# Kernel optimization log

Measured on AMD Instinct MI355X. Metric: run time of the kernel, lower is better.

The kernel has to match this reference:

```python
import jax, jax.numpy as jnp
import numpy as np

B, H, W = 16, 256, 256
C = 64          # width
M1, M2 = 12, 12 # retained Fourier modes
FC_HID = 128


def setup_inputs() -> dict:
    key = jax.random.key(0)
    ks = jax.random.split(key, 10)
    scale = 1.0 / (C * C)
    inp = {
        "x": jax.random.normal(ks[0], (B, H, W, 1), dtype=jnp.float32),
        "fc0_w": jax.random.normal(ks[1], (1, C), dtype=jnp.float32) * (1.0 / np.sqrt(1)),
        "fc0_b": jnp.zeros((C,), dtype=jnp.float32),
        # 4 layers x {weights1, weights2} x [Cin, Cout, M1, M2] x {re, im}
        "sc_w": jax.random.uniform(ks[2], (4, 2, C, C, M1, M2, 2), dtype=jnp.float32) * scale,
        # 1x1 conv weights [layer, Cout, Cin] and biases [layer, Cout]
        "pw_w": jax.random.normal(ks[3], (4, C, C), dtype=jnp.float32) * (1.0 / np.sqrt(C)),
        "pw_b": jnp.zeros((4, C), dtype=jnp.float32),
        "fc1_w": jax.random.normal(ks[4], (C, FC_HID), dtype=jnp.float32) * (1.0 / np.sqrt(C)),
        "fc1_b": jnp.zeros((FC_HID,), dtype=jnp.float32),
        "fc2_w": jax.random.normal(ks[5], (FC_HID, 1), dtype=jnp.float32) * (1.0 / np.sqrt(FC_HID)),
        "fc2_b": jnp.zeros((1,), dtype=jnp.float32),
    }
    return inp


def _spectral_conv(x, w1, w2):
    # x: [B, C, H, W] real; w1, w2: [Cin, Cout, M1, M2] complex
    xf = jnp.fft.rfft2(x, axes=(-2, -1))                # [B, C, H, W//2+1]
    top = jnp.einsum('bixy,ioxy->boxy', xf[:, :, :M1, :M2], w1)
    bot = jnp.einsum('bixy,ioxy->boxy', xf[:, :, -M1:, :M2], w2)
    out_ft = jnp.zeros((x.shape[0], w1.shape[1], x.shape[2], x.shape[3] // 2 + 1),
                       dtype=jnp.complex64)
    out_ft = out_ft.at[:, :, :M1, :M2].set(top)
    out_ft = out_ft.at[:, :, -M1:, :M2].set(bot)
    return jnp.fft.irfft2(out_ft, s=(x.shape[2], x.shape[3]), axes=(-2, -1))


def _gelu(x):
    return jax.nn.gelu(x, approximate=False)  # torch F.gelu default = exact erf


def reference(x, fc0_w, fc0_b, sc_w, pw_w, pw_b, fc1_w, fc1_b, fc2_w, fc2_b):
    # lift: [B,H,W,1] -> [B,H,W,C] -> [B,C,H,W]
    h = jnp.einsum('bhwi,ic->bhwc', x, fc0_w) + fc0_b
    h = jnp.transpose(h, (0, 3, 1, 2))
    scw = sc_w[..., 0] + 1j * sc_w[..., 1]  # [4, 2, C, C, M1, M2] complex
    for l in range(4):
        x1 = _spectral_conv(h, scw[l, 0], scw[l, 1])
        x2 = jnp.einsum('bihw,oi->bohw', h, pw_w[l]) + pw_b[l][None, :, None, None]
        h = x1 + x2
        if l < 3:
            h = _gelu(h)
    h = jnp.transpose(h, (0, 2, 3, 1))  # [B,H,W,C]
    h = _gelu(jnp.einsum('bhwc,cd->bhwd', h, fc1_w) + fc1_b)
    out = jnp.einsum('bhwd,do->bhwo', h, fc2_w) + fc2_b
    return out
```

## Files before the change

### kernel.cpp

```cpp
#include <hip/hip_runtime.h>
#include <hip/hip_bf16.h>
#include <math.h>

#define Hn 256
#define Wn 256
#define Cn 64
#define Mk 12
#define NM 24
#define FCH 128
#define HW 65536

using half8 = __attribute__((ext_vector_type(8))) _Float16;
using f32x4 = __attribute__((ext_vector_type(4))) float;

__device__ __forceinline__ float gelu_exact(float x) {
    return 0.5f * x * (1.0f + erff(x * 0.7071067811865476f));
}
__device__ __forceinline__ unsigned short f2h(float f) {
    _Float16 h = (_Float16)f;
    return __builtin_bit_cast(unsigned short, h);
}
__device__ __forceinline__ float h2lo(unsigned u) {
    return (float)__builtin_bit_cast(_Float16, (unsigned short)(u & 0xffffu));
}
__device__ __forceinline__ float h2hi(unsigned u) {
    return (float)__builtin_bit_cast(_Float16, (unsigned short)(u >> 16));
}

__global__ __launch_bounds__(256) void k_init_tables(float* tc, float* ts,
                                                     float* twc, float* tws,
                                                     float* tcs,
                                                     unsigned short* bfr,
                                                     unsigned short* tfr) {
    int i = threadIdx.x;
    const float step = 0.024543692606170259f;
    float c = cosf(i * step), s = sinf(i * step);
    tc[i] = c; ts[i] = s;
    tcs[2 * i] = c; tcs[2 * i + 1] = s;
    for (int k = 0; k < Mk; ++k) {
        int idx = (i * k) & 255;
        twc[i * Mk + k] = cosf(idx * step);
        tws[i * Mk + k] = sinf(idx * step);
    }
    for (int e = i; e < 8192; e += 256) {
        int j  = e & 7;
        int l  = (e >> 3) & 63;
        int sn = e >> 9;
        int col = (sn & 1) * 16 + (l & 15);
        int ky = col >> 1, p = col & 1;
        int k  = (sn >> 1) * 32 + ((l >> 4) & 3) * 8 + j;
        int idx = (ky * k) & 255;
        float v = p ? -sinf(idx * step) : cosf(idx * step);
        bfr[e] = f2h(v);
    }
    for (int e = i; e < 12288; e += 256) {
        int j  = e & 7;
        int l  = (e >> 3) & 63;
        int sm = e >> 9;
        int mt = sm % 3, s2 = sm / 3;
        int r  = mt * 16 + (l & 15);
        int hh = s2 * 32 + ((l >> 4) & 3) * 8 + j;
        int m  = (r < 24) ? r : (r - 24);
        int kx = (m < Mk) ? m : (232 + m);
        int idx = (kx * hh) & 255;
        float v = (r < 24) ? cosf(idx * step) : sinf(idx * step);
        tfr[e] = f2h(v);
    }
}

__global__ __launch_bounds__(256) void k_prep_frag(const float* __restrict__ pww,
                                                   const float* __restrict__ fc1w,
                                                   unsigned short* __restrict__ efr,
                                                   unsigned short* __restrict__ pwfr,
                                                   unsigned short* __restrict__ fc1fr) {
    int e = blockIdx.x * 256 + threadIdx.x;
    const float step = 0.024543692606170259f;
    int j = e & 7, l = (e >> 3) & 63;
    int row = l & 15;
    int k = ((l >> 4) & 3) * 8 + j;
    if (e < 8192) {
        int mt = (e >> 9) & 15;
        int pix = mt * 16 + row;
        float v = 0.f;
        if (k < 12) v = cosf(((k * pix) & 255) * step);
        else if (k < 24) v = -sinf((((k - 12) * pix) & 255) * step);
        efr[e] = f2h(v);
    } else if (e < 24576) {
        int e2 = e - 8192;
        int nt = (e2 >> 9) & 3;
        int ks = (e2 >> 11) & 1;
        int l4 = e2 >> 12;
        int o = nt * 16 + row;
        int i = ks * 32 + k;
        pwfr[e2] = f2h(pww[(size_t)(l4 * 64 + o) * 64 + i]);
    } else {
        int e2 = e - 24576;
        int nt = (e2 >> 9) & 7;
        int ks = (e2 >> 12) & 1;
        int d = nt * 16 + row;
        int i = ks * 32 + k;
        fc1fr[e2] = f2h(fc1w[i * 128 + d]);
    }
}

__global__ __launch_bounds__(256) void k_prep_w(const float* __restrict__ scw,
                                                float* __restrict__ scwT) {
    int t = blockIdx.x * 256 + threadIdx.x;
    int o  = t & 63;
    int i  = (t >> 6) & 63;
    int r  = t >> 12;
    int u  = r % 6;
    int kx = (r / 6) % 12;
    int lj = r / 72;
    int ky = 2 * u;
    size_t in_idx = ((((size_t)lj * 64 + i) * 64 + o) * 144) + kx * Mk + ky;
    float4 v = *(const float4*)(scw + 2 * in_idx);
    size_t o0 = ((((size_t)(lj * 12 + kx) * Mk + ky) * 64 + i) * 64 + o);
    size_t o1 = ((((size_t)(lj * 12 + kx) * Mk + ky + 1) * 64 + i) * 64 + o);
    *(float2*)(scwT + 2 * o0) = make_float2(v.x, v.y);
    *(float2*)(scwT + 2 * o1) = make_float2(v.z, v.w);
}

__global__ __launch_bounds__(256) void k_prep_wfrag(const float* __restrict__ scwT,
                                                    unsigned short* __restrict__ wfr) {
    __shared__ float Ws[8192];
    int mat = blockIdx.x;
    int t = threadIdx.x;
    const float4* src = (const float4*)(scwT + (size_t)mat * 8192);
#pragma unroll
    for (int r = 0; r < 8; ++r)
        ((float4*)Ws)[r * 256 + t] = src[r * 256 + t];
    __syncthreads();
    unsigned short* dst = wfr + (size_t)mat * 16384;
#pragma unroll
    for (int u = 0; u < 8; ++u) {
        int lin = u * 256 + t;
        int lane = lin & 63, nt = (lin >> 6) & 7, s = lin >> 9;
        int col = nt * 16 + (lane & 15);
        int o = col >> 1, pp = col & 1;
        int tg = (lane >> 4) & 3;
        unsigned pk[4];
#pragma unroll
        for (int jp = 0; jp < 4; ++jp) {
            unsigned short hv[2];
#pragma unroll
            for (int hz = 0; hz < 2; ++hz) {
                int k = s * 32 + tg * 8 + jp * 2 + hz;
                int i = k >> 1, p = k & 1;
                float wr_ = Ws[(i * 64 + o) * 2];
                float wi_ = Ws[(i * 64 + o) * 2 + 1];
                float v = (p == 0) ? (pp == 0 ? wr_ : wi_)
                                   : (pp == 0 ? -wi_ : wr_);
                hv[hz] = f2h(v);
            }
            pk[jp] = hv[0] | ((unsigned)hv[1] << 16);
        }
        uint4 w4 = {pk[0], pk[1], pk[2], pk[3]};
        *(uint4*)(dst + lin * 8) = w4;
    }
}

__global__ __launch_bounds__(64) void k_dftw_x(const float* __restrict__ x,
                                               float* __restrict__ Xxw,
                                               const float* __restrict__ twc,
                                               const float* __restrict__ tws) {
    int r = blockIdx.x * 64 + threadIdx.x;
    const float* hp = x + (size_t)r * Wn;
    float xr[Mk], xi[Mk];
#pragma unroll
    for (int k = 0; k < Mk; ++k) { xr[k] = 0.f; xi[k] = 0.f; }
    for (int w4 = 0; w4 < 64; ++w4) {
        float4 v = ((const float4*)hp)[w4];
        float vv[4] = {v.x, v.y, v.z, v.w};
#pragma unroll
        for (int j = 0; j < 4; ++j) {
            int wbase = (w4 * 4 + j) * Mk;
#pragma unroll
            for (int k = 0; k < Mk; ++k) {
                xr[k] += vv[j] * twc[wbase + k];
                xi[k] -= vv[j] * tws[wbase + k];
            }
        }
    }
    float* op = Xxw + (size_t)r * (2 * Mk);
#pragma unroll
    for (int k = 0; k < Mk; ++k) { op[2 * k] = xr[k]; op[2 * k + 1] = xi[k]; }
}

__global__ __launch_bounds__(256) void k_xdfth(const float* __restrict__ Xxw,
                                               float* __restrict__ Xfx,
                                               const float* __restrict__ tc,
                                               const float* __restrict__ ts) {
    int t = blockIdx.x * 256 + threadIdx.x;
    if (t >= 16 * 288) return;
    int ky = t % Mk;
    int m  = (t / Mk) % NM;
    int b  = t / 288;
    int kx = (m < Mk) ? m : (232 + m);
    const float* base = Xxw + (size_t)b * Hn * 2 * Mk + 2 * ky;
    float ar = 0.f, ai = 0.f;
    for (int hh = 0; hh < Hn; ++hh) {
        float vr = base[hh * 2 * Mk];
        float vi = base[hh * 2 * Mk + 1];
        int idx = (kx * hh) & 255;
        float c = tc[idx], s = ts[idx];
        ar += vr * c + vi * s;
        ai += vi * c - vr * s;
    }
    Xfx[2 * t] = ar;
    Xfx[2 * t + 1] = ai;
}

__global__ __launch_bounds__(256) void k_mixZ2(const float* __restrict__ xin,
                                               const unsigned short* __restrict__ wfr,
                                               const float* __restrict__ w0,
                                               const float* __restrict__ b0v,
                                               float* __restrict__ Z,
                                               int l, int first, int b0, int bc) {
    __shared__ __align__(16) char smem[4096];
    int t = threadIdx.x;
    int lane = t & 63, q = t >> 6, tg = (lane >> 4) & 3;
    int blk = blockIdx.x;
    int jj = blk / 144, kxw = (blk / 12) % 12, ky = blk % 12;
    int mm = jj * 12 + kxw;
    int mk = mm * 12 + ky;
    int mat = (l * 2 + jj) * 144 + kxw * 12 + ky;
    {
        int b = t >> 4, c16 = t & 15;
        uint4 pk = {0u, 0u, 0u, 0u};
        if (b < bc) {
            if (first) {
                float xr = xin[((b0 + b) * 288 + mk) * 2] * 0.0625f;
                float xi = xin[((b0 + b) * 288 + mk) * 2 + 1] * 0.0625f;
                float4 wv = *(const float4*)(w0 + c16 * 4);
                float4 bv = {0.f, 0.f, 0.f, 0.f};
                if (mk == 0) {
                    float4 bb = *(const float4*)(b0v + c16 * 4);
                    bv.x = 4096.f * bb.x; bv.y = 4096.f * bb.y;
                    bv.z = 4096.f * bb.z; bv.w = 4096.f * bb.w;
                }
                pk.x = f2h(wv.x * xr + bv.x) | ((unsigned)f2h(wv.x * xi) << 16);
                pk.y = f2h(wv.y * xr + bv.y) | ((unsigned)f2h(wv.y * xi) << 16);
                pk.z = f2h(wv.z * xr + bv.z) | ((unsigned)f2h(wv.z * xi) << 16);
                pk.w = f2h(wv.w * xr + bv.w) | ((unsigned)f2h(wv.w * xi) << 16);
            } else {
                const float* src = xin + ((size_t)b * 288 + mk) * 128 + c16 * 8;
                float4 v0 = *(const float4*)(src);
                float4 v1 = *(const float4*)(src + 4);
                pk.x = f2h(v0.x * 0.0625f) | ((unsigned)f2h(v0.y * 0.0625f) << 16);
                pk.y = f2h(v0.z * 0.0625f) | ((unsigned)f2h(v0.w * 0.0625f) << 16);
                pk.z = f2h(v1.x * 0.0625f) | ((unsigned)f2h(v1.y * 0.0625f) << 16);
                pk.w = f2h(v1.z * 0.0625f) | ((unsigned)f2h(v1.w * 0.0625f) << 16);
            }
        }
        *(uint4*)(smem + ((b * 256 + c16 * 16) ^ ((b & 7) << 4))) = pk;
    }
    __syncthreads();
    const uint4* bt = (const uint4*)wfr + (size_t)mat * 2048;
    f32x4 ac0 = {0.f, 0.f, 0.f, 0.f};
    f32x4 ac1 = {0.f, 0.f, 0.f, 0.f};
    int brow = lane & 15;
#pragma unroll
    for (int s = 0; s < 4; ++s) {
        half8 af = *(const half8*)(smem + ((brow * 256 + s * 64 + tg * 16) ^ ((brow & 7) << 4)));
        half8 bf0 = __builtin_bit_cast(half8, bt[(s * 8 + 2 * q) * 64 + lane]);
        half8 bf1 = __builtin_bit_cast(half8, bt[(s * 8 + 2 * q + 1) * 64 + lane]);
        ac0 = __builtin_amdgcn_mfma_f32_16x16x32_f16(af, bf0, ac0, 0, 0, 0);
        ac1 = __builtin_amdgcn_mfma_f32_16x16x32_f16(af, bf1, ac1, 0, 0, 0);
    }
    const float sc = 16.0f * 2.0f / 65536.0f;
#pragma unroll
    for (int n = 0; n < 2; ++n) {
        f32x4 ac = n ? ac1 : ac0;
        int col = (2 * q + n) * 16 + (lane & 15);
        int o = col >> 1, pp = col & 1;
#pragma unroll
        for (int r = 0; r < 4; ++r) {
            int bb = (lane >> 4) * 4 + r;
            if (bb < bc)
                Z[(((size_t)bb * 12 + ky) * 64 + o) * 48 + mm * 2 + pp] = ac[r] * sc;
        }
    }
}

__global__ __launch_bounds__(256) void k_dfth(const float* __restrict__ Xw,
                                              float* __restrict__ Xf2,
                                              const unsigned short* __restrict__ tfr) {
    __shared__ __align__(16) char smem[65536];
    int b = blockIdx.x / 12, ky = blockIdx.x % 12;
    int t = threadIdx.x;
    int lane = t & 63, q = t >> 6;
    const float* P = Xw + ((size_t)b * 12 + ky) * 32768;
    int c = lane;
#pragma unroll 4
    for (int k = 0; k < 32; ++k) {
        int hh0 = k * 8 + q * 2;
        float2 a  = *(const float2*)(P + hh0 * 128 + 2 * c);
        float2 bv = *(const float2*)(P + (hh0 + 1) * 128 + 2 * c);
        unsigned int u0 = f2h(a.x * 0.0625f) | ((unsigned int)f2h(bv.x * 0.0625f) << 16);
        unsigned int u1 = f2h(a.y * 0.0625f) | ((unsigned int)f2h(bv.y * 0.0625f) << 16);
        int ch0 = 2 * c, ch1 = 2 * c + 1;
        *(unsigned int*)(smem + ch0 * 512 + ((2 * hh0) ^ ((ch0 & 7) << 4))) = u0;
        *(unsigned int*)(smem + ch1 * 512 + ((2 * hh0) ^ ((ch1 & 7) << 4))) = u1;
    }
    __syncthreads();
    int ct0 = q * 2;
    int tg = (lane >> 4) & 3;
    f32x4 a00 = {0,0,0,0}, a01 = {0,0,0,0}, a10 = {0,0,0,0};
    f32x4 a11 = {0,0,0,0}, a20 = {0,0,0,0}, a21 = {0,0,0,0};
    const uint4* tf4 = (const uint4*)tfr;
#pragma unroll
    for (int s = 0; s < 8; ++s) {
        half8 af0 = __builtin_bit_cast(half8, tf4[(s * 3 + 0) * 64 + lane]);
        half8 af1 = __builtin_bit_cast(half8, tf4[(s * 3 + 1) * 64 + lane]);
        half8 af2 = __builtin_bit_cast(half8, tf4[(s * 3 + 2) * 64 + lane]);
        int chan0 = ct0 * 16 + (lane & 15);
        int chan1 = chan0 + 16;
        int off = s * 64 + tg * 16;
        half8 b0 = *(const half8*)(smem + chan0 * 512 + (off ^ ((chan0 & 7) << 4)));
        half8 b1 = *(const half8*)(smem + chan1 * 512 + (off ^ ((chan1 & 7) << 4)));
        a00 = __builtin_amdgcn_mfma_f32_16x16x32_f16(af0, b0, a00, 0, 0, 0);
        a01 = __builtin_amdgcn_mfma_f32_16x16x32_f16(af0, b1, a01, 0, 0, 0);
        a10 = __builtin_amdgcn_mfma_f32_16x16x32_f16(af1, b0, a10, 0, 0, 0);
        a11 = __builtin_amdgcn_mfma_f32_16x16x32_f16(af1, b1, a11, 0, 0, 0);
        a20 = __builtin_amdgcn_mfma_f32_16x16x32_f16(af2, b0, a20, 0, 0, 0);
        a21 = __builtin_amdgcn_mfma_f32_16x16x32_f16(af2, b1, a21, 0, 0, 0);
    }
    __syncthreads();
    float* Cs = (float*)smem;
    {
        int rl = (lane >> 4) * 4;
        int chan0 = ct0 * 16 + (lane & 15);
#pragma unroll
        for (int r = 0; r < 4; ++r) {
            Cs[(0  + rl + r) * 128 + chan0]      = a00[r];
            Cs[(0  + rl + r) * 128 + chan0 + 16] = a01[r];
            Cs[(16 + rl + r) * 128 + chan0]      = a10[r];
            Cs[(16 + rl + r) * 128 + chan0 + 16] = a11[r];
            Cs[(32 + rl + r) * 128 + chan0]      = a20[r];
            Cs[(32 + rl + r) * 128 + chan0 + 16] = a21[r];
        }
    }
    __syncthreads();
#pragma unroll
    for (int k = 0; k < 6; ++k) {
        int p = t + 256 * k;
        int m = p >> 6, i = p & 63;
        float r1 = Cs[m * 128 + 2 * i];
        float i1 = Cs[m * 128 + 2 * i + 1];
        float r2 = Cs[(24 + m) * 128 + 2 * i];
        float i2 = Cs[(24 + m) * 128 + 2 * i + 1];
        ((float2*)Xf2)[((size_t)b * 288 + m * 12 + ky) * 64 + i] =
            make_float2((r1 + i2) * 16.0f, (i1 - r2) * 16.0f);
    }
}

__global__ __launch_bounds__(256, 4) void k_fusedA(const float* xh,
        const float* __restrict__ Zb, const float* __restrict__ pwb,
        const float* __restrict__ w0, const float* __restrict__ b0v,
        float* hn, float* __restrict__ XwOut,
        const float* __restrict__ tcs,
        const unsigned short* __restrict__ bfr,
        const unsigned short* __restrict__ efr,
        const unsigned short* __restrict__ pwfr,
        int l, int first) {
    __shared__ __align__(16) char smem[37120];
    float* Ysh = (float*)smem;
    char*  Yfr = smem + 32768;
    float* csm = (float*)(smem + 36864);
    int b  = blockIdx.x >> 8;
    int hh = blockIdx.x & 255;
    int w  = threadIdx.x;
    int lane = w & 63, q = w >> 6;
    int tg = (lane >> 4) & 3;
    const float2* tc2 = (const float2*)tcs;
    if (w < NM) {
        int kx = (w < Mk) ? w : (232 + w);
        float2 cs = tc2[(kx * hh) & 255];
        csm[2 * w] = cs.x; csm[2 * w + 1] = cs.y;
    }
    __syncthreads();
    const float* Zbb = Zb + (size_t)b * 36864;
    const float4* cs4 = (const float4*)csm;
#pragma unroll
    for (int r3 = 0; r3 < 3; ++r3) {
        int p = w + 256 * r3;
        int o = p / Mk, ky = p % Mk;
        const float4* zv = (const float4*)(Zbb + ((size_t)ky * 64 + o) * 48);
        float yr = 0.f, yi = 0.f;
#pragma unroll
        for (int mm = 0; mm < 12; ++mm) {
            float4 z  = zv[mm];
            float4 cc = cs4[mm];
            yr += z.x * cc.x - z.y * cc.y + z.z * cc.z - z.w * cc.w;
            yi += z.x * cc.y + z.y * cc.x + z.z * cc.w + z.w * cc.z;
        }
        Ysh[p * 2] = yr; Ysh[p * 2 + 1] = yi;
    }
    __syncthreads();
    {
        int o = q * 16 + (lane & 15);
        unsigned pv[4];
#pragma unroll
        for (int jp = 0; jp < 4; ++jp) {
            unsigned short h2[2];
#pragma unroll
            for (int hzz = 0; hzz < 2; ++hzz) {
                int u = tg * 8 + jp * 2 + hzz;
                float v;
                if (u == 0) v = 0.5f * Ysh[o * 24];
                else if (u < 12) v = Ysh[o * 24 + 2 * u];
                else if (u < 24) v = Ysh[o * 24 + 2 * (u - 12) + 1];
                else v = 0.f;
                h2[hzz] = f2h(v);
            }
            pv[jp] = h2[0] | ((unsigned)h2[1] << 16);
        }
        uint4 pk = {pv[0], pv[1], pv[2], pv[3]};
        *(uint4*)(Yfr + (q * 64 + lane) * 16) = pk;
    }
    __syncthreads();
    {
        int swz = (w & 7) << 4;
        if (first) {
            float xv = xh[(size_t)b * HW + hh * 256 + w];
#pragma unroll
            for (int ic = 0; ic < 4; ++ic) {
                unsigned pv[8];
#pragma unroll
                for (int j2 = 0; j2 < 16; j2 += 2) {
                    float a0 = w0[ic * 16 + j2] * xv + b0v[ic * 16 + j2];
                    float a1 = w0[ic * 16 + j2 + 1] * xv + b0v[ic * 16 + j2 + 1];
                    pv[j2 >> 1] = f2h(a0) | ((unsigned)f2h(a1) << 16);
                }
                uint4 lo = {pv[0], pv[1], pv[2], pv[3]};
                uint4 hi = {pv[4], pv[5], pv[6], pv[7]};
                *(uint4*)(smem + ((w * 128 + ic * 32) ^ swz)) = lo;
                *(uint4*)(smem + ((w * 128 + ic * 32 + 16) ^ swz)) = hi;
            }
        } else {
            const float* hb = xh + (size_t)b * Cn * HW + hh * 256 + w;
#pragma unroll
            for (int ic = 0; ic < 4; ++ic) {
                unsigned pv[8];
#pragma unroll
                for (int j2 = 0; j2 < 16; j2 += 2) {
                    float a0 = hb[(size_t)(ic * 16 + j2) * HW];
                    float a1 = hb[(size_t)(ic * 16 + j2 + 1) * HW];
                    pv[j2 >> 1] = f2h(a0) | ((unsigned)f2h(a1) << 16);
                }
                uint4 lo = {pv[0], pv[1], pv[2], pv[3]};
                uint4 hi = {pv[4], pv[5], pv[6], pv[7]};
                *(uint4*)(smem + ((w * 128 + ic * 32) ^ swz)) = lo;
                *(uint4*)(smem + ((w * 128 + ic * 32 + 16) ^ swz)) = hi;
            }
        }
    }
    __syncthreads();
    uint2 gp[4][4];
    {
        const uint4* efr4 = (const uint4*)efr;
        const uint4* pw4  = (const uint4*)pwfr;
        float biasn[4];
        half8 ybf[4]; uint4 cwa[4], cwb[4];
#pragma unroll
        for (int nt = 0; nt < 4; ++nt) {
            biasn[nt] = pwb[l * 64 + nt * 16 + (lane & 15)];
            ybf[nt] = *(const half8*)(Yfr + (nt * 64 + lane) * 16);
            cwa[nt] = pw4[((l * 2 + 0) * 4 + nt) * 64 + lane];
            cwb[nt] = pw4[((l * 2 + 1) * 4 + nt) * 64 + lane];
        }
#pragma unroll
        for (int mt = 0; mt < 4; ++mt) {
            int mtA = q * 4 + mt;
            half8 ea = __builtin_bit_cast(half8, efr4[mtA * 64 + lane]);
            int row = mtA * 16 + (lane & 15);
            int rsw = (row & 7) << 4;
            half8 a0 = *(const half8*)(smem + ((row * 128 + tg * 16) ^ rsw));
            half8 a1 = *(const half8*)(smem + ((row * 128 + 64 + tg * 16) ^ rsw));
#pragma unroll
            for (int nt = 0; nt < 4; ++nt) {
                f32x4 acc = {0.f, 0.f, 0.f, 0.f};
                acc = __builtin_amdgcn_mfma_f32_16x16x32_f16(ea, ybf[nt], acc, 0, 0, 0);
                acc = __builtin_amdgcn_mfma_f32_16x16x32_f16(a0, __builtin_bit_cast(half8, cwa[nt]), acc, 0, 0, 0);
                acc = __builtin_amdgcn_mfma_f32_16x16x32_f16(a1, __builtin_bit_cast(half8, cwb[nt]), acc, 0, 0, 0);
                float g0 = gelu_exact(acc[0] + biasn[nt]);
                float g1 = gelu_exact(acc[1] + biasn[nt]);
                float g2 = gelu_exact(acc[2] + biasn[nt]);
                float g3 = gelu_exact(acc[3] + biasn[nt]);
                gp[mt][nt].x = f2h(g0) | ((unsigned)f2h(g1) << 16);
                gp[mt][nt].y = f2h(g2) | ((unsigned)f2h(g3) << 16);
            }
        }
    }
    float* hnb = hn + (size_t)b * Cn * HW + hh * 256;
#pragma unroll
    for (int mt = 0; mt < 4; ++mt) {
        int pbase = (q * 4 + mt) * 16 + (lane >> 4) * 4;
#pragma unroll
        for (int nt = 0; nt < 4; ++nt) {
            int o = nt * 16 + (lane & 15);
            uint2 g2 = gp[mt][nt];
            float4 hv = {h2lo(g2.x), h2hi(g2.x), h2lo(g2.y), h2hi(g2.y)};
            *(float4*)(hnb + (size_t)o * HW + pbase) = hv;
        }
    }
    __syncthreads();
#pragma unroll
    for (int mt = 0; mt < 4; ++mt) {
        int pbase = (q * 4 + mt) * 16 + (lane >> 4) * 4;
#pragma unroll
        for (int nt = 0; nt < 4; ++nt) {
            int o = nt * 16 + (lane & 15);
            int sidx = (((pbase >> 3) ^ (o & 7)) << 3) | (pbase & 7);
            *(uint2*)(smem + o * 512 + sidx * 2) = gp[mt][nt];
        }
    }
    __syncthreads();
    {
        int arow = q * 16 + (lane & 15);
        const uint4* bt = (const uint4*)bfr;
        f32x4 ac0 = {0.f, 0.f, 0.f, 0.f};
        f32x4 ac1 = {0.f, 0.f, 0.f, 0.f};
#pragma unroll
        for (int s = 0; s < 8; ++s) {
            int abyte = (arow * 512 + s * 64 + tg * 16) ^ ((arow & 7) << 4);
            half8 af = __builtin_bit_cast(half8, *(const uint4*)(smem + abyte));
            half8 b0 = __builtin_bit_cast(half8, bt[(s * 2 + 0) * 64 + lane]);
            half8 b1 = __builtin_bit_cast(half8, bt[(s * 2 + 1) * 64 + lane]);
            ac0 = __builtin_amdgcn_mfma_f32_16x16x32_f16(af, b0, ac0, 0, 0, 0);
            ac1 = __builtin_amdgcn_mfma_f32_16x16x32_f16(af, b1, ac1, 0, 0, 0);
        }
        float* Xwb = XwOut + (size_t)b * 393216;
        int rbase = q * 16 + (lane >> 4) * 4;
#pragma unroll
        for (int n = 0; n < 2; ++n) {
            f32x4 ac = n ? ac1 : ac0;
            int col = n * 16 + (lane & 15);
            int ky = col >> 1, p = col & 1;
            if (ky < Mk) {
                float* dst = Xwb + (size_t)ky * 32768 + hh * 128 + rbase * 2 + p;
                dst[0] = ac[0]; dst[2] = ac[1]; dst[4] = ac[2]; dst[6] = ac[3];
            }
        }
    }
}

__global__ __launch_bounds__(256, 4) void k_fusedB(const float* __restrict__ h,
        const float* __restrict__ Zb, const float* __restrict__ pwb,
        const float* __restrict__ fc1b, const float* __restrict__ fc2w,
        const float* __restrict__ fc2b, float* __restrict__ outp,
        const float* __restrict__ tcs,
        const unsigned short* __restrict__ efr,
        const unsigned short* __restrict__ pwfr,
        const unsigned short* __restrict__ fc1fr) {
    __shared__ __align__(16) char smem[37120];
    float* Ysh = (float*)smem;
    char*  Yfr = smem + 32768;
    float* csm = (float*)(smem + 36864);
    int b  = blockIdx.x >> 8;
    int hh = blockIdx.x & 255;
    int w  = threadIdx.x;
    int lane = w & 63, q = w >> 6;
    int tg = (lane >> 4) & 3;
    const float2* tc2 = (const float2*)tcs;
    if (w < NM) {
        int kx = (w < Mk) ? w : (232 + w);
        float2 cs = tc2[(kx * hh) & 255];
        csm[2 * w] = cs.x; csm[2 * w + 1] = cs.y;
    }
    __syncthreads();
    const float* Zbb = Zb + (size_t)b * 36864;
    const float4* cs4 = (const float4*)csm;
#pragma unroll
    for (int r3 = 0; r3 < 3; ++r3) {
        int p = w + 256 * r3;
        int o = p / Mk, ky = p % Mk;
        const float4* zv = (const float4*)(Zbb + ((size_t)ky * 64 + o) * 48);
        float yr = 0.f, yi = 0.f;
#pragma unroll
        for (int mm = 0; mm < 12; ++mm) {
            float4 z  = zv[mm];
            float4 cc = cs4[mm];
            yr += z.x * cc.x - z.y * cc.y + z.z * cc.z - z.w * cc.w;
            yi += z.x * cc.y + z.y * cc.x + z.z * cc.w + z.w * cc.z;
        }
        Ysh[p * 2] = yr; Ysh[p * 2 + 1] = yi;
    }
    __syncthreads();
    {
        int o = q * 16 + (lane & 15);
        unsigned pv[4];
#pragma unroll
        for (int jp = 0; jp < 4; ++jp) {
            unsigned short h2[2];
#pragma unroll
            for (int hzz = 0; hzz < 2; ++hzz) {
                int u = tg * 8 + jp * 2 + hzz;
                float v;
                if (u == 0) v = 0.5f * Ysh[o * 24];
                else if (u < 12) v = Ysh[o * 24 + 2 * u];
                else if (u < 24) v = Ysh[o * 24 + 2 * (u - 12) + 1];
                else v = 0.f;
                h2[hzz] = f2h(v);
            }
            pv[jp] = h2[0] | ((unsigned)h2[1] << 16);
        }
        uint4 pk = {pv[0], pv[1], pv[2], pv[3]};
        *(uint4*)(Yfr + (q * 64 + lane) * 16) = pk;
    }
    __syncthreads();
    {
        int swz = (w & 7) << 4;
        const float* hb = h + (size_t)b * Cn * HW + hh * 256 + w;
#pragma unroll
        for (int ic = 0; ic < 4; ++ic) {
            unsigned pv[8];
#pragma unroll
            for (int j2 = 0; j2 < 16; j2 += 2) {
                float a0 = hb[(size_t)(ic * 16 + j2) * HW];
                float a1 = hb[(size_t)(ic * 16 + j2 + 1) * HW];
                pv[j2 >> 1] = f2h(a0) | ((unsigned)f2h(a1) << 16);
            }
            uint4 lo = {pv[0], pv[1], pv[2], pv[3]};
            uint4 hi = {pv[4], pv[5], pv[6], pv[7]};
            *(uint4*)(smem + ((w * 128 + ic * 32) ^ swz)) = lo;
            *(uint4*)(smem + ((w * 128 + ic * 32 + 16) ^ swz)) = hi;
        }
    }
    __syncthreads();
    uint2 R2[16];
    {
        const uint4* efr4 = (const uint4*)efr;
        const uint4* pw4 = (const uint4*)pwfr;
        half8 ay  = *(const half8*)(Yfr + (q * 64 + lane) * 16);
        half8 aw0 = __builtin_bit_cast(half8, pw4[((3 * 2 + 0) * 4 + q) * 64 + lane]);
        half8 aw1 = __builtin_bit_cast(half8, pw4[((3 * 2 + 1) * 4 + q) * 64 + lane]);
        int obase = q * 16 + (lane >> 4) * 4;
        float4 bias4 = *(const float4*)(pwb + 3 * 64 + obase);
#pragma unroll
        for (int nt = 0; nt < 16; ++nt) {
            half8 eb = __builtin_bit_cast(half8, efr4[nt * 64 + lane]);
            int pix = nt * 16 + (lane & 15);
            int psw = (pix & 7) << 4;
            half8 b0 = *(const half8*)(smem + ((pix * 128 + tg * 16) ^ psw));
            half8 b1 = *(const half8*)(smem + ((pix * 128 + 64 + tg * 16) ^ psw));
            f32x4 acc = {0.f, 0.f, 0.f, 0.f};
            acc = __builtin_amdgcn_mfma_f32_16x16x32_f16(ay, eb, acc, 0, 0, 0);
            acc = __builtin_amdgcn_mfma_f32_16x16x32_f16(aw0, b0, acc, 0, 0, 0);
            acc = __builtin_amdgcn_mfma_f32_16x16x32_f16(aw1, b1, acc, 0, 0, 0);
            R2[nt].x = f2h(acc[0] + bias4.x) | ((unsigned)f2h(acc[1] + bias4.y) << 16);
            R2[nt].y = f2h(acc[2] + bias4.z) | ((unsigned)f2h(acc[3] + bias4.w) << 16);
        }
    }
    __syncthreads();
    {
        int obase = q * 16 + (lane >> 4) * 4;
#pragma unroll
        for (int nt = 0; nt < 16; ++nt) {
            int pix = nt * 16 + (lane & 15);
            *(uint2*)(smem + ((pix * 128 + obase * 2) ^ ((pix & 7) << 4))) = R2[nt];
        }
    }
    __syncthreads();
    const uint4* f14 = (const uint4*)fc1fr;
    float w2v[8], fb1[8];
#pragma unroll
    for (int nt = 0; nt < 8; ++nt) {
        w2v[nt] = fc2w[nt * 16 + (lane & 15)];
        fb1[nt] = fc1b[nt * 16 + (lane & 15)];
    }
    float fb = fc2b[0];
    float* ob = outp + (size_t)b * HW + hh * 256;
#pragma unroll
    for (int mt = 0; mt < 4; ++mt) {
        int mtA = q * 4 + mt;
        int row = mtA * 16 + (lane & 15);
        int rsw = (row & 7) << 4;
        half8 a0 = *(const half8*)(smem + ((row * 128 + tg * 16) ^ rsw));
        half8 a1 = *(const half8*)(smem + ((row * 128 + 64 + tg * 16) ^ rsw));
        float s0 = 0.f, s1 = 0.f, s2 = 0.f, s3 = 0.f;
#pragma unroll
        for (int nt = 0; nt < 8; ++nt) {
            f32x4 acc = {0.f, 0.f, 0.f, 0.f};
            acc = __builtin_amdgcn_mfma_f32_16x16x32_f16(a0, __builtin_bit_cast(half8, f14[(0 * 8 + nt) * 64 + lane]), acc, 0, 0, 0);
            acc = __builtin_amdgcn_mfma_f32_16x16x32_f16(a1, __builtin_bit_cast(half8, f14[(1 * 8 + nt) * 64 + lane]), acc, 0, 0, 0);
            s0 += gelu_exact(acc[0] + fb1[nt]) * w2v[nt];
            s1 += gelu_exact(acc[1] + fb1[nt]) * w2v[nt];
            s2 += gelu_exact(acc[2] + fb1[nt]) * w2v[nt];
            s3 += gelu_exact(acc[3] + fb1[nt]) * w2v[nt];
        }
#pragma unroll
        for (int msk = 1; msk <= 8; msk <<= 1) {
            s0 += __shfl_xor(s0, msk);
            s1 += __shfl_xor(s1, msk);
            s2 += __shfl_xor(s2, msk);
            s3 += __shfl_xor(s3, msk);
        }
        int cc = lane & 15;
        if (cc < 4) {
            float v = (cc == 0) ? s0 : (cc == 1) ? s1 : (cc == 2) ? s2 : s3;
            ob[mtA * 16 + (lane >> 4) * 4 + cc] = v + fb;
        }
    }
}

extern "C" void kernel_launch(void* const* d_in, const int* in_sizes, int n_in,
                              void* d_out, int out_size, void* d_ws, size_t ws_size,
                              hipStream_t stream) {
    const float* x    = (const float*)d_in[0];
    const float* fc0w = (const float*)d_in[1];
    const float* fc0b = (const float*)d_in[2];
    const float* scw  = (const float*)d_in[3];
    const float* pww  = (const float*)d_in[4];
    const float* pwb  = (const float*)d_in[5];
    const float* fc1w = (const float*)d_in[6];
    const float* fc1b = (const float*)d_in[7];
    const float* fc2w = (const float*)d_in[8];
    const float* fc2b = (const float*)d_in[9];
    float* out = (float*)d_out;
    float* ws  = (float*)d_ws;

    const size_t basef = 18917376;
    const size_t perbf = 4661248;
    int bc = 0;
    for (int cand = 16; cand >= 1; cand >>= 1)
        if ((basef + perbf * (size_t)cand) * 4 <= ws_size) { bc = cand; break; }
    if (bc == 0) return;

    float* tabc = ws;
    float* tabs = tabc + 256;
    float* twc  = tabs + 256;
    float* tws_ = twc + 3072;
    float* tcs  = tws_ + 3072;
    float* bfr  = tcs + 512;
    float* tfr  = bfr + 4096;
    float* efr  = tfr + 6144;
    float* pwfr = efr + 4096;
    float* fc1f = pwfr + 8192;
    float* Xfx  = fc1f + 4096;
    float* scwT = Xfx + 9216;
    float* wfr  = scwT + 9437184;
    float* hbuf = ws + basef;
    float* Xw   = hbuf + (size_t)bc * 4194304;
    float* Zb   = Xw + (size_t)bc * 393216;
    float* Xf2  = Zb + (size_t)bc * 36864;

    k_init_tables<<<1, 256, 0, stream>>>(tabc, tabs, twc, tws_, tcs,
                                         (unsigned short*)bfr,
                                         (unsigned short*)tfr);
    k_prep_frag<<<128, 256, 0, stream>>>(pww, fc1w,
                                         (unsigned short*)efr,
                                         (unsigned short*)pwfr,
                                         (unsigned short*)fc1f);
    k_prep_w<<<9216, 256, 0, stream>>>(scw, scwT);
    k_prep_wfrag<<<1152, 256, 0, stream>>>(scwT, (unsigned short*)wfr);
    k_dftw_x<<<64, 64, 0, stream>>>(x, hbuf, twc, tws_);
    k_xdfth<<<18, 256, 0, stream>>>(hbuf, Xfx, tabc, tabs);

    for (int b0 = 0; b0 < 16; b0 += bc) {
        k_mixZ2<<<288, 256, 0, stream>>>(Xfx, (const unsigned short*)wfr,
                                         fc0w, fc0b, Zb, 0, 1, b0, bc);
        k_fusedA<<<bc * 256, 256, 0, stream>>>(x + (size_t)b0 * HW, Zb, pwb,
                                               fc0w, fc0b, hbuf, Xw, tcs,
                                               (const unsigned short*)bfr,
                                               (const unsigned short*)efr,
                                               (const unsigned short*)pwfr, 0, 1);
        for (int l = 1; l <= 2; ++l) {
            k_dfth<<<bc * 12, 256, 0, stream>>>(Xw, Xf2, (const unsigned short*)tfr);
            k_mixZ2<<<288, 256, 0, stream>>>(Xf2, (const unsigned short*)wfr,
                                             fc0w, fc0b, Zb, l, 0, b0, bc);
            k_fusedA<<<bc * 256, 256, 0, stream>>>(hbuf, Zb, pwb,
                                                   fc0w, fc0b, hbuf, Xw, tcs,
                                                   (const unsigned short*)bfr,
                                                   (const unsigned short*)efr,
                                                   (const unsigned short*)pwfr, l, 0);
        }
        k_dfth<<<bc * 12, 256, 0, stream>>>(Xw, Xf2, (const unsigned short*)tfr);
        k_mixZ2<<<288, 256, 0, stream>>>(Xf2, (const unsigned short*)wfr,
                                         fc0w, fc0b, Zb, 3, 0, b0, bc);
        k_fusedB<<<bc * 256, 256, 0, stream>>>(hbuf, Zb, pwb, fc1b, fc2w, fc2b,
                                               out + (size_t)b0 * HW, tcs,
                                               (const unsigned short*)efr,
                                               (const unsigned short*)pwfr,
                                               (const unsigned short*)fc1f);
    }
}
```

Before: 1.605 ms.

## Store hidden activations as fp16, fuse weight prep, split mixZ2 blocks

Hidden activations between layers are now stored as fp16 instead of fp32. Since they were already rounded to fp16 before the MFMA, this halves activation write and read traffic in the fused kernels. The separate weight-transpose kernel is removed, and fragment prep now gathers directly from the original spectral weights with strided loads. The mixZ2 grid is doubled so each wave computes one N-tile instead of two, giving more parallelism at the cost of reloading the A tile per block. A smaller workspace may also allow larger batch chunks.

Result: no change. 1.577 ms (-1.7%).

```diff
diff --git a/kernel.cpp b/kernel.cpp
--- a/kernel.cpp
+++ b/kernel.cpp
@@ -19,12 +19,6 @@
 __device__ __forceinline__ unsigned short f2h(float f) {
     _Float16 h = (_Float16)f;
     return __builtin_bit_cast(unsigned short, h);
-}
-__device__ __forceinline__ float h2lo(unsigned u) {
-    return (float)__builtin_bit_cast(_Float16, (unsigned short)(u & 0xffffu));
-}
-__device__ __forceinline__ float h2hi(unsigned u) {
-    return (float)__builtin_bit_cast(_Float16, (unsigned short)(u >> 16));
 }
 
 __global__ __launch_bounds__(256) void k_init_tables(float* tc, float* ts,
@@ -103,33 +97,19 @@
     }
 }
 
-__global__ __launch_bounds__(256) void k_prep_w(const float* __restrict__ scw,
-                                                float* __restrict__ scwT) {
-    int t = blockIdx.x * 256 + threadIdx.x;
-    int o  = t & 63;
-    int i  = (t >> 6) & 63;
-    int r  = t >> 12;
-    int u  = r % 6;
-    int kx = (r / 6) % 12;
-    int lj = r / 72;
-    int ky = 2 * u;
-    size_t in_idx = ((((size_t)lj * 64 + i) * 64 + o) * 144) + kx * Mk + ky;
-    float4 v = *(const float4*)(scw + 2 * in_idx);
-    size_t o0 = ((((size_t)(lj * 12 + kx) * Mk + ky) * 64 + i) * 64 + o);
-    size_t o1 = ((((size_t)(lj * 12 + kx) * Mk + ky + 1) * 64 + i) * 64 + o);
-    *(float2*)(scwT + 2 * o0) = make_float2(v.x, v.y);
-    *(float2*)(scwT + 2 * o1) = make_float2(v.z, v.w);
-}
-
-__global__ __launch_bounds__(256) void k_prep_wfrag(const float* __restrict__ scwT,
+__global__ __launch_bounds__(256) void k_prep_wfrag(const float* __restrict__ scw,
                                                     unsigned short* __restrict__ wfr) {
     __shared__ float Ws[8192];
     int mat = blockIdx.x;
+    int lj = mat / 144, kxw = (mat / 12) % 12, ky = mat % 12;
     int t = threadIdx.x;
-    const float4* src = (const float4*)(scwT + (size_t)mat * 8192);
-#pragma unroll
-    for (int r = 0; r < 8; ++r)
-        ((float4*)Ws)[r * 256 + t] = src[r * 256 + t];
+    const float* base = scw + (((size_t)lj * 4096) * 144 + kxw * 12 + ky) * 2;
+#pragma unroll
+    for (int r = 0; r < 16; ++r) {
+        int idx = r * 256 + t;
+        float2 v = *(const float2*)(base + (size_t)idx * 288);
+        Ws[idx * 2] = v.x; Ws[idx * 2 + 1] = v.y;
+    }
     __syncthreads();
     unsigned short* dst = wfr + (size_t)mat * 16384;
 #pragma unroll
@@ -220,7 +200,9 @@
     __shared__ __align__(16) char smem[4096];
     int t = threadIdx.x;
     int lane = t & 63, q = t >> 6, tg = (lane >> 4) & 3;
-    int blk = blockIdx.x;
+    int blk2 = blockIdx.x;
+    int hlf = blk2 & 1;
+    int blk = blk2 >> 1;
     int jj = blk / 144, kxw = (blk / 12) % 12, ky = blk % 12;
     int mm = jj * 12 + kxw;
     int mk = mm * 12 + ky;
@@ -256,30 +238,24 @@
         *(uint4*)(smem + ((b * 256 + c16 * 16) ^ ((b & 7) << 4))) = pk;
     }
     __syncthreads();
+    int nt = hlf * 4 + q;
     const uint4* bt = (const uint4*)wfr + (size_t)mat * 2048;
-    f32x4 ac0 = {0.f, 0.f, 0.f, 0.f};
-    f32x4 ac1 = {0.f, 0.f, 0.f, 0.f};
+    f32x4 ac = {0.f, 0.f, 0.f, 0.f};
     int brow = lane & 15;
 #pragma unroll
     for (int s = 0; s < 4; ++s) {
         half8 af = *(const half8*)(smem + ((brow * 256 + s * 64 + tg * 16) ^ ((brow & 7) << 4)));
-        half8 bf0 = __builtin_bit_cast(half8, bt[(s * 8 + 2 * q) * 64 + lane]);
-        half8 bf1 = __builtin_bit_cast(half8, bt[(s * 8 + 2 * q + 1) * 64 + lane]);
-        ac0 = __builtin_amdgcn_mfma_f32_16x16x32_f16(af, bf0, ac0, 0, 0, 0);
-        ac1 = __builtin_amdgcn_mfma_f32_16x16x32_f16(af, bf1, ac1, 0, 0, 0);
+        half8 bf = __builtin_bit_cast(half8, bt[(s * 8 + nt) * 64 + lane]);
+        ac = __builtin_amdgcn_mfma_f32_16x16x32_f16(af, bf, ac, 0, 0, 0);
     }
     const float sc = 16.0f * 2.0f / 65536.0f;
-#pragma unroll
-    for (int n = 0; n < 2; ++n) {
-        f32x4 ac = n ? ac1 : ac0;
-        int col = (2 * q + n) * 16 + (lane & 15);
-        int o = col >> 1, pp = col & 1;
-#pragma unroll
-        for (int r = 0; r < 4; ++r) {
-            int bb = (lane >> 4) * 4 + r;
-            if (bb < bc)
-                Z[(((size_t)bb * 12 + ky) * 64 + o) * 48 + mm * 2 + pp] = ac[r] * sc;
-        }
+    int col = nt * 16 + (lane & 15);
+    int o = col >> 1, pp = col & 1;
+#pragma unroll
+    for (int r = 0; r < 4; ++r) {
+        int bb = (lane >> 4) * 4 + r;
+        if (bb < bc)
+            Z[(((size_t)bb * 12 + ky) * 64 + o) * 48 + mm * 2 + pp] = ac[r] * sc;
     }
 }
 
@@ -355,10 +331,11 @@
     }
 }
 
-__global__ __launch_bounds__(256, 4) void k_fusedA(const float* xh,
+__global__ __launch_bounds__(256, 4) void k_fusedA(const float* __restrict__ x0,
+        const unsigned short* hin,
         const float* __restrict__ Zb, const float* __restrict__ pwb,
         const float* __restrict__ w0, const float* __restrict__ b0v,
-        float* hn, float* __restrict__ XwOut,
+        unsigned short* hout, float* __restrict__ XwOut,
         const float* __restrict__ tcs,
         const unsigned short* __restrict__ bfr,
         const unsigned short* __restrict__ efr,
@@ -423,7 +400,7 @@
     {
         int swz = (w & 7) << 4;
         if (first) {
-            float xv = xh[(size_t)b * HW + hh * 256 + w];
+            float xv = x0[(size_t)b * HW + hh * 256 + w];
 #pragma unroll
             for (int ic = 0; ic < 4; ++ic) {
                 unsigned pv[8];
@@ -439,15 +416,15 @@
                 *(uint4*)(smem + ((w * 128 + ic * 32 + 16) ^ swz)) = hi;
             }
         } else {
-            const float* hb = xh + (size_t)b * Cn * HW + hh * 256 + w;
+            const unsigned short* hb = hin + (size_t)b * Cn * HW + hh * 256 + w;
 #pragma unroll
             for (int ic = 0; ic < 4; ++ic) {
                 unsigned pv[8];
 #pragma unroll
                 for (int j2 = 0; j2 < 16; j2 += 2) {
-                    float a0 = hb[(size_t)(ic * 16 + j2) * HW];
-                    float a1 = hb[(size_t)(ic * 16 + j2 + 1) * HW];
-                    pv[j2 >> 1] = f2h(a0) | ((unsigned)f2h(a1) << 16);
+                    unsigned a0 = hb[(size_t)(ic * 16 + j2) * HW];
+                    unsigned a1 = hb[(size_t)(ic * 16 + j2 + 1) * HW];
+                    pv[j2 >> 1] = a0 | (a1 << 16);
                 }
                 uint4 lo = {pv[0], pv[1], pv[2], pv[3]};
                 uint4 hi = {pv[4], pv[5], pv[6], pv[7]};
@@ -493,16 +470,14 @@
             }
         }
     }
-    float* hnb = hn + (size_t)b * Cn * HW + hh * 256;
+    unsigned short* hnb = hout + (size_t)b * Cn * HW + hh * 256;
 #pragma unroll
     for (int mt = 0; mt < 4; ++mt) {
         int pbase = (q * 4 + mt) * 16 + (lane >> 4) * 4;
 #pragma unroll
         for (int nt = 0; nt < 4; ++nt) {
             int o = nt * 16 + (lane & 15);
-            uint2 g2 = gp[mt][nt];
-            float4 hv = {h2lo(g2.x), h2hi(g2.x), h2lo(g2.y), h2hi(g2.y)};
-            *(float4*)(hnb + (size_t)o * HW + pbase) = hv;
+            *(uint2*)(hnb + (size_t)o * HW + pbase) = gp[mt][nt];
         }
     }
     __syncthreads();
@@ -546,7 +521,7 @@
     }
 }
 
-__global__ __launch_bounds__(256, 4) void k_fusedB(const float* __restrict__ h,
+__global__ __launch_bounds__(256, 4) void k_fusedB(const unsigned short* __restrict__ hin,
         const float* __restrict__ Zb, const float* __restrict__ pwb,
         const float* __restrict__ fc1b, const float* __restrict__ fc2w,
         const float* __restrict__ fc2b, float* __restrict__ outp,
@@ -612,15 +587,15 @@
     __syncthreads();
     {
         int swz = (w & 7) << 4;
-        const float* hb = h + (size_t)b * Cn * HW + hh * 256 + w;
+        const unsigned short* hb = hin + (size_t)b * Cn * HW + hh * 256 + w;
 #pragma unroll
         for (int ic = 0; ic < 4; ++ic) {
             unsigned pv[8];
 #pragma unroll
             for (int j2 = 0; j2 < 16; j2 += 2) {
-                float a0 = hb[(size_t)(ic * 16 + j2) * HW];
-                float a1 = hb[(size_t)(ic * 16 + j2 + 1) * HW];
-                pv[j2 >> 1] = f2h(a0) | ((unsigned)f2h(a1) << 16);
+                unsigned a0 = hb[(size_t)(ic * 16 + j2) * HW];
+                unsigned a1 = hb[(size_t)(ic * 16 + j2 + 1) * HW];
+                pv[j2 >> 1] = a0 | (a1 << 16);
             }
             uint4 lo = {pv[0], pv[1], pv[2], pv[3]};
             uint4 hi = {pv[4], pv[5], pv[6], pv[7]};
@@ -721,8 +696,8 @@
     float* out = (float*)d_out;
     float* ws  = (float*)d_ws;
 
-    const size_t basef = 18917376;
-    const size_t perbf = 4661248;
+    const size_t basef = 9578496;
+    const size_t perbf = 2564096;
     int bc = 0;
     for (int cand = 16; cand >= 1; cand >>= 1)
         if ((basef + perbf * (size_t)cand) * 4 <= ws_size) { bc = cand; break; }
@@ -739,10 +714,11 @@
     float* pwfr = efr + 4096;
     float* fc1f = pwfr + 8192;
     float* Xfx  = fc1f + 4096;
-    float* scwT = Xfx + 9216;
-    float* wfr  = scwT + 9437184;
+    float* wfr  = Xfx + 9216;
+    float* Xxw  = wfr + 9437184;
     float* hbuf = ws + basef;
-    float* Xw   = hbuf + (size_t)bc * 4194304;
+    unsigned short* h16 = (unsigned short*)hbuf;
+    float* Xw   = hbuf + (size_t)bc * 2097152;
     float* Zb   = Xw + (size_t)bc * 393216;
     float* Xf2  = Zb + (size_t)bc * 36864;
 
@@ -753,33 +729,32 @@
                                          (unsigned short*)efr,
                                          (unsigned short*)pwfr,
                                          (unsigned short*)fc1f);
-    k_prep_w<<<9216, 256, 0, stream>>>(scw, scwT);
-    k_prep_wfrag<<<1152, 256, 0, stream>>>(scwT, (unsigned short*)wfr);
-    k_dftw_x<<<64, 64, 0, stream>>>(x, hbuf, twc, tws_);
-    k_xdfth<<<18, 256, 0, stream>>>(hbuf, Xfx, tabc, tabs);
+    k_prep_wfrag<<<1152, 256, 0, stream>>>(scw, (unsigned short*)wfr);
+    k_dftw_x<<<64, 64, 0, stream>>>(x, Xxw, twc, tws_);
+    k_xdfth<<<18, 256, 0, stream>>>(Xxw, Xfx, tabc, tabs);
 
     for (int b0 = 0; b0 < 16; b0 += bc) {
-        k_mixZ2<<<288, 256, 0, stream>>>(Xfx, (const unsigned short*)wfr,
+        k_mixZ2<<<576, 256, 0, stream>>>(Xfx, (const unsigned short*)wfr,
                                          fc0w, fc0b, Zb, 0, 1, b0, bc);
-        k_fusedA<<<bc * 256, 256, 0, stream>>>(x + (size_t)b0 * HW, Zb, pwb,
-                                               fc0w, fc0b, hbuf, Xw, tcs,
+        k_fusedA<<<bc * 256, 256, 0, stream>>>(x + (size_t)b0 * HW, h16, Zb, pwb,
+                                               fc0w, fc0b, h16, Xw, tcs,
                                                (const unsigned short*)bfr,
                                                (const unsigned short*)efr,
                                                (const unsigned short*)pwfr, 0, 1);
         for (int l = 1; l <= 2; ++l) {
             k_dfth<<<bc * 12, 256, 0, stream>>>(Xw, Xf2, (const unsigned short*)tfr);
-            k_mixZ2<<<288, 256, 0, stream>>>(Xf2, (const unsigned short*)wfr,
+            k_mixZ2<<<576, 256, 0, stream>>>(Xf2, (const unsigned short*)wfr,
                                              fc0w, fc0b, Zb, l, 0, b0, bc);
-            k_fusedA<<<bc * 256, 256, 0, stream>>>(hbuf, Zb, pwb,
-                                                   fc0w, fc0b, hbuf, Xw, tcs,
+            k_fusedA<<<bc * 256, 256, 0, stream>>>(x, h16, Zb, pwb,
+                                                   fc0w, fc0b, h16, Xw, tcs,
                                                    (const unsigned short*)bfr,
                                                    (const unsigned short*)efr,
                                                    (const unsigned short*)pwfr, l, 0);
         }
         k_dfth<<<bc * 12, 256, 0, stream>>>(Xw, Xf2, (const unsigned short*)tfr);
-        k_mixZ2<<<288, 256, 0, stream>>>(Xf2, (const unsigned short*)wfr,
+        k_mixZ2<<<576, 256, 0, stream>>>(Xf2, (const unsigned short*)wfr,
                                          fc0w, fc0b, Zb, 3, 0, b0, bc);
-        k_fusedB<<<bc * 256, 256, 0, stream>>>(hbuf, Zb, pwb, fc1b, fc2w, fc2b,
+        k_fusedB<<<bc * 256, 256, 0, stream>>>(h16, Zb, pwb, fc1b, fc2w, fc2b,
                                                out + (size_t)b0 * HW, tcs,
                                                (const unsigned short*)efr,
                                                (const unsigned short*)pwfr,
```
